# Kernel optimization log

Hardware: AMD Instinct MI355X
Metric: run time of the kernel (lower is better)

Reference implementation:

```python
import jax, jax.numpy as jnp
import numpy as np
from jax import lax

B, INP, OUP, H, W = 16, 128, 128, 56, 56
EXPAND = 6
HID = INP * EXPAND  # 768
EPS = 1e-5


def setup_inputs() -> dict:
    key = jax.random.key(0)
    ks = jax.random.split(key, 18)
    x = jax.random.normal(ks[0], (B, INP, H, W), dtype=jnp.float32)
    mask = jax.random.randint(ks[1], (B, 1, H, W), 0, 2, dtype=jnp.int32)
    w1 = jax.random.normal(ks[2], (HID, INP), dtype=jnp.float32) * 0.05
    g1 = 1.0 + 0.1 * jax.random.normal(ks[3], (HID,), dtype=jnp.float32)
    b1 = 0.1 * jax.random.normal(ks[4], (HID,), dtype=jnp.float32)
    m1 = 0.1 * jax.random.normal(ks[5], (HID,), dtype=jnp.float32)
    v1 = jax.random.uniform(ks[6], (HID,), dtype=jnp.float32) + 0.5
    wdw = jax.random.normal(ks[7], (HID, 1, 3, 3), dtype=jnp.float32) * 0.05
    g2 = 1.0 + 0.1 * jax.random.normal(ks[8], (HID,), dtype=jnp.float32)
    b2 = 0.1 * jax.random.normal(ks[9], (HID,), dtype=jnp.float32)
    m2 = 0.1 * jax.random.normal(ks[10], (HID,), dtype=jnp.float32)
    v2 = jax.random.uniform(ks[11], (HID,), dtype=jnp.float32) + 0.5
    w2 = jax.random.normal(ks[12], (OUP, HID), dtype=jnp.float32) * 0.05
    g3 = 1.0 + 0.1 * jax.random.normal(ks[13], (OUP,), dtype=jnp.float32)
    b3 = 0.1 * jax.random.normal(ks[14], (OUP,), dtype=jnp.float32)
    m3 = 0.1 * jax.random.normal(ks[15], (OUP,), dtype=jnp.float32)
    v3 = jax.random.uniform(ks[16], (OUP,), dtype=jnp.float32) + 0.5
    return dict(x=x, w1=w1, g1=g1, b1=b1, m1=m1, v1=v1, wdw=wdw,
                g2=g2, b2=b2, m2=m2, v2=v2, w2=w2,
                g3=g3, b3=b3, m3=m3, v3=v3, mask=mask)


def _bn(h, g, b, m, v):
    # inference-mode BatchNorm2d: (h - mean) * gamma/sqrt(var+eps) + beta
    scale = g / jnp.sqrt(v + EPS)
    return (h - m[None, :, None, None]) * scale[None, :, None, None] + b[None, :, None, None]


def reference(x, w1, g1, b1, m1, v1, wdw, g2, b2, m2, v2, w2, g3, b3, m3, v3, mask):
    mf = mask.astype(x.dtype)  # [B,1,H,W] binary mask ('std')
    # mask_dilate: 3x3 binary dilation (dilate_stride=1) so the depthwise conv
    # has valid neighbors for every active output pixel
    md = lax.reduce_window(mf, 0.0, lax.max, (1, 1, 3, 3), (1, 1, 1, 1), 'SAME')
    # expand 1x1 conv + BN + ReLU6, restricted to dilated mask
    h = jnp.einsum('bchw,kc->bkhw', x, w1)            # [B,HID,H,W]
    h = jnp.clip(_bn(h, g1, b1, m1, v1), 0.0, 6.0) * md
    # depthwise 3x3 conv + BN + ReLU6, restricted to std mask
    h = lax.conv_general_dilated(h, wdw, (1, 1), 'SAME',
                                 feature_group_count=HID,
                                 dimension_numbers=('NCHW', 'OIHW', 'NCHW'))
    h = jnp.clip(_bn(h, g2, b2, m2, v2), 0.0, 6.0) * mf
    # project 1x1 conv + BN (no relu), restricted to std mask
    h = jnp.einsum('bkhw,ok->bohw', h, w2)            # [B,OUP,H,W]
    h = _bn(h, g3, b3, m3, v3) * mf
    # scatter-add into identity path
    return x + h
```

## Files before the change

### kernel.cpp

```cpp
#include <hip/hip_runtime.h>
#include <hip/hip_bf16.h>

#define BATCH 16
#define INP   128
#define OUP   128
#define HH    56
#define WW    56
#define HWSZ  3136
#define HID   768
#define EPSV  1e-5f

#define SCPD  63
#define RWST  (32 * SCPD)
#define H2STR 72

typedef __attribute__((ext_vector_type(8))) short bf16x8;
typedef __attribute__((ext_vector_type(4))) float f32x4;
typedef __attribute__((ext_vector_type(2))) float f32x2;

__device__ __forceinline__ unsigned short f2b(float f) {
    unsigned u = __float_as_uint(f);
    return (unsigned short)((u + 0x7FFFu + ((u >> 16) & 1u)) >> 16);
}
__device__ __forceinline__ float blo(unsigned u){ return __uint_as_float(u << 16); }
__device__ __forceinline__ float bhi(unsigned u){ return __uint_as_float(u & 0xFFFF0000u); }
__device__ __forceinline__ unsigned pkbf(float lo, float hi) {
    unsigned r;
    asm("v_cvt_pk_bf16_f32 %0, %1, %2" : "=v"(r) : "v"(lo), "v"(hi));
    return r;
}
__device__ __forceinline__ void pkfma(f32x2& a, f32x2 b, f32x2 c) {
    asm("v_pk_fma_f32 %0, %1, %2, %0" : "+v"(a) : "v"(b), "v"(c));
}

__global__ void prep(const float* __restrict__ w1, const float* __restrict__ g1,
                     const float* __restrict__ b1, const float* __restrict__ m1, const float* __restrict__ v1,
                     const float* __restrict__ wdw, const float* __restrict__ g2,
                     const float* __restrict__ b2, const float* __restrict__ m2, const float* __restrict__ v2,
                     const float* __restrict__ w2, const float* __restrict__ g3,
                     const float* __restrict__ b3, const float* __restrict__ m3, const float* __restrict__ v3,
                     const int* __restrict__ mask,
                     unsigned short* __restrict__ w1f, unsigned short* __restrict__ w2f,
                     float* __restrict__ be1o, float* __restrict__ wdsf,
                     float* __restrict__ be2o, float* __restrict__ be3o,
                     float* __restrict__ mdf, float* __restrict__ mff)
{
    int gid = blockIdx.x * blockDim.x + threadIdx.x;
    int stp = gridDim.x * blockDim.x;
    for (int i = gid; i < HID * INP; i += stp) {
        int r = i >> 7, k = i & 127;
        float s = g1[r] * rsqrtf(v1[r] + EPSV);
        int ht = r >> 4, r16 = r & 15, ks = k >> 5, g = (k >> 3) & 3, e = k & 7;
        w1f[((((ht * 4 + ks) * 4 + g) * 16 + r16) << 3) + e] = f2b(w1[i] * s);
    }
    for (int i = gid; i < OUP * HID; i += stp) {
        int r = i / HID, k = i - r * HID;
        float s = g3[r] * rsqrtf(v3[r] + EPSV);
        int ot = r >> 4, r16 = r & 15, ch = k >> 6, ks = (k >> 5) & 1, g = (k >> 3) & 3, e = k & 7;
        int lane = g * 16 + r16;
        w2f[((((ot * 12 + ch) * 2 + ks) * 64 + lane) << 3) + e] = f2b(w2[i] * s);
    }
    for (int i = gid; i < HID; i += stp) {
        float s1 = g1[i] * rsqrtf(v1[i] + EPSV);
        be1o[i] = b1[i] - m1[i] * s1;
        float s2 = g2[i] * rsqrtf(v2[i] + EPSV);
        be2o[i] = b2[i] - m2[i] * s2;
    }
    for (int i = gid; i < HID * 9; i += stp) {
        int q = i / HID, c = i - q * HID;
        float s2 = g2[c] * rsqrtf(v2[c] + EPSV);
        wdsf[i] = wdw[c * 9 + q] * s2;
    }
    for (int i = gid; i < OUP; i += stp) {
        float s3 = g3[i] * rsqrtf(v3[i] + EPSV);
        be3o[i] = b3[i] - m3[i] * s3;
    }
    for (int i = gid; i < BATCH * HWSZ; i += stp) {
        int b = i / HWSZ, p = i - b * HWSZ;
        int y = p / WW, xx = p - y * WW;
        float mf = (float)mask[i];
        float md = 0.f;
        for (int dy = -1; dy <= 1; ++dy)
            for (int dx = -1; dx <= 1; ++dx) {
                int yy = y + dy, xc = xx + dx;
                if (yy >= 0 && yy < HH && xc >= 0 && xc < WW)
                    md = fmaxf(md, (float)mask[b * HWSZ + yy * WW + xc]);
            }
        mff[i] = mf;
        mdf[i] = md;
    }
}

__launch_bounds__(512, 4)
__global__ void k1_expand(const float* __restrict__ x,
                          const unsigned short* __restrict__ w1f,
                          const float* __restrict__ be1g,
                          const float* __restrict__ mdf,
                          unsigned* __restrict__ h1p)
{
    __shared__ unsigned short xs[128 * 128];
    const int t = threadIdx.x, lane = t & 63, wv = t >> 6;
    const int g = lane >> 4, r16 = lane & 15;
    const int pid = blockIdx.x;
    const int l = (pid & 7) * 150 + (pid >> 3);
    const int hb = l % 3;
    const int pb = (l / 3) % 25;
    const int b  = l / 75;
    const int p0 = pb * 128;
    const int whid = wv & 3;
    const int wpx  = wv >> 2;

    for (int rep = 0; rep < 8; ++rep) {
        int id = t + rep * 512;
        int px = id & 127, c4 = id >> 7;
        int p = p0 + px;
        ushort4 u; u.x = 0; u.y = 0; u.z = 0; u.w = 0;
        if (p < HWSZ) {
            const float* xp = x + ((size_t)(b * INP + c4 * 4)) * HWSZ + p;
            unsigned lo = pkbf(xp[0], xp[HWSZ]);
            unsigned hi = pkbf(xp[2 * HWSZ], xp[3 * HWSZ]);
            u.x = (unsigned short)lo; u.y = (unsigned short)(lo >> 16);
            u.z = (unsigned short)hi; u.w = (unsigned short)(hi >> 16);
        }
        *(ushort4*)&xs[px * 128 + (((c4 >> 1) ^ (px & 15)) << 3) + ((c4 & 1) << 2)] = u;
    }
    __syncthreads();

    f32x4 acc[4][4];
    #pragma unroll
    for (int mt = 0; mt < 4; ++mt)
        #pragma unroll
        for (int nt = 0; nt < 4; ++nt) {
            acc[mt][nt][0] = 0.f; acc[mt][nt][1] = 0.f;
            acc[mt][nt][2] = 0.f; acc[mt][nt][3] = 0.f;
        }
    const int hbase = hb * 256 + whid * 64;
    const int htb = hbase >> 4;

    #pragma unroll
    for (int ks = 0; ks < 4; ++ks) {
        bf16x8 af[4];
        #pragma unroll
        for (int mt = 0; mt < 4; ++mt)
            af[mt] = *(const bf16x8*)&w1f[((((htb + mt) * 4 + ks) * 64) + lane) << 3];
        #pragma unroll
        for (int nt = 0; nt < 4; ++nt) {
            int px = wpx * 64 + nt * 16 + r16;
            bf16x8 bf = *(const bf16x8*)&xs[px * 128 + (((ks * 4 + g) ^ r16) << 3)];
            #pragma unroll
            for (int mt = 0; mt < 4; ++mt)
                acc[mt][nt] = __builtin_amdgcn_mfma_f32_16x16x32_bf16(af[mt], bf, acc[mt][nt], 0, 0, 0);
        }
    }

    #pragma unroll
    for (int nt = 0; nt < 4; ++nt) {
        const int pg = p0 + wpx * 64 + nt * 16;
        if (pg >= HWSZ) continue;
        const int p = pg + r16;
        const float md = mdf[b * HWSZ + p];
        #pragma unroll
        for (int mt = 0; mt < 4; ++mt) {
            const float4 be4 = *(const float4*)&be1g[hbase + mt * 16 + g * 4];
            f32x4 a = acc[mt][nt];
            float v0 = fminf(fmaxf(a[0] + be4.x, 0.f), 6.f) * md;
            float v1 = fminf(fmaxf(a[1] + be4.y, 0.f), 6.f) * md;
            float v2 = fminf(fmaxf(a[2] + be4.z, 0.f), 6.f) * md;
            float v3 = fminf(fmaxf(a[3] + be4.w, 0.f), 6.f) * md;
            const int c2 = (hbase >> 1) + mt * 8 + g * 2;
            const size_t ad = (size_t)(b * 384 + c2) * HWSZ + p;
            h1p[ad] = pkbf(v0, v1);
            h1p[ad + HWSZ] = pkbf(v2, v3);
        }
    }
}

__launch_bounds__(512, 4)
__global__ void k23(const unsigned* __restrict__ h1p,
                    const unsigned short* __restrict__ w2f,
                    const float* __restrict__ wdsf,
                    const float* __restrict__ be2g,
                    const float* __restrict__ be3g,
                    const float* __restrict__ mff,
                    const float* __restrict__ x,
                    float* __restrict__ out)
{
    __shared__ unsigned stg[4 * RWST];
    __shared__ unsigned short h2s[112 * H2STR];
    __shared__ float mfv_[112];

    const int t = threadIdx.x, lane = t & 63, wv = t >> 6;
    const int g = lane >> 4, r16 = lane & 15;
    const int pid = blockIdx.x;
    const int l = (pid & 7) * 56 + (pid >> 3);
    const int strip = l % 28, b = l / 28;
    const int y0 = strip * 2, p0 = strip * 112;

    if (t < 112) mfv_[t] = mff[b * HWSZ + p0 + t];
    if (t >= 128 && t < 384) {
        int i = t - 128;
        int cp = i & 31, rs = (i >> 5) & 3, side = (i >> 7) & 1;
        stg[rs * RWST + cp * SCPD + (side ? 58 : 1)] = 0;
    }

    int gaddr[4], laddr[4]; bool gval[4], wval[4];
    #pragma unroll
    for (int rep = 0; rep < 4; ++rep) {
        const int id = t + rep * 512;
        const int rr  = (id * 4682) >> 16;
        const int px4 = id - rr * 14;
        const int row = rr & 3, cp = rr >> 2;
        const int gy = y0 - 1 + row;
        wval[rep] = id < 1792;
        gval[rep] = wval[rep] && gy >= 0 && gy < HH;
        gaddr[rep] = (b * 384 + cp) * HWSZ + gy * WW + px4 * 4;
        laddr[rep] = row * RWST + cp * SCPD + 2 + px4 * 4;
    }
    uint4 sreg[4];

    auto issueLoads = [&]() {
        #pragma unroll
        for (int rep = 0; rep < 4; ++rep) {
            uint4 u; u.x = 0; u.y = 0; u.z = 0; u.w = 0;
            if (gval[rep]) u = *(const uint4*)&h1p[gaddr[rep]];
            sreg[rep] = u;
            gaddr[rep] += 32 * HWSZ;
        }
    };
    auto stageWrite = [&]() {
        #pragma unroll
        for (int rep = 0; rep < 4; ++rep) {
            if (wval[rep]) {
                unsigned* s = &stg[laddr[rep]];
                s[0] = sreg[rep].x; s[1] = sreg[rep].y;
                s[2] = sreg[rep].z; s[3] = sreg[rep].w;
            }
        }
    };

    const int cp_c = t & 31, row2 = (t >> 5) & 1, q = t >> 6;
    unsigned* const h2d = (unsigned*)h2s;

    auto phaseDW = [&](int ch) {
        f32x2 acc2[7];
        {
            const float2 be2 = *(const float2*)&be2g[ch * 64 + 2 * cp_c];
            #pragma unroll
            for (int j = 0; j < 7; ++j) { acc2[j][0] = be2.x; acc2[j][1] = be2.y; }
        }
        #pragma unroll
        for (int dy = 0; dy < 3; ++dy) {
            f32x2 wt0 = *(const f32x2*)&wdsf[(dy * 3 + 0) * HID + ch * 64 + 2 * cp_c];
            f32x2 wt1 = *(const f32x2*)&wdsf[(dy * 3 + 1) * HID + ch * 64 + 2 * cp_c];
            f32x2 wt2 = *(const f32x2*)&wdsf[(dy * 3 + 2) * HID + ch * 64 + 2 * cp_c];
            const unsigned* rp = &stg[(row2 + dy) * RWST + cp_c * SCPD + 1 + q * 7];
            f32x2 p[9];
            #pragma unroll
            for (int k = 0; k < 9; ++k) {
                unsigned u = rp[k];
                p[k][0] = blo(u); p[k][1] = bhi(u);
            }
            #pragma unroll
            for (int j = 0; j < 7; ++j) {
                pkfma(acc2[j], p[j], wt0);
                pkfma(acc2[j], p[j + 1], wt1);
                pkfma(acc2[j], p[j + 2], wt2);
            }
        }
        #pragma unroll
        for (int j = 0; j < 7; ++j) {
            const int px = row2 * 56 + q * 7 + j;
            const float mv = mfv_[px];
            float vL = __builtin_amdgcn_fmed3f(acc2[j][0], 0.f, 6.f) * mv;
            float vH = __builtin_amdgcn_fmed3f(acc2[j][1], 0.f, 6.f) * mv;
            h2d[px * 36 + (((cp_c >> 2) ^ (px & 7)) << 2) + (cp_c & 3)] = pkbf(vL, vH);
        }
    };

    f32x4 pacc[7];
    #pragma unroll
    for (int nt = 0; nt < 7; ++nt) {
        pacc[nt][0] = 0.f; pacc[nt][1] = 0.f; pacc[nt][2] = 0.f; pacc[nt][3] = 0.f;
    }

    auto phaseP = [&](int ch) {
        #pragma unroll
        for (int ks = 0; ks < 2; ++ks) {
            const bf16x8 pw = *(const bf16x8*)&w2f[((((wv * 12 + ch) * 2 + ks) * 64) + lane) << 3];
            #pragma unroll
            for (int nt = 0; nt < 7; ++nt) {
                const int px = nt * 16 + r16;
                const bf16x8 hb = *(const bf16x8*)&h2s[px * H2STR + (((ks * 4 + g) ^ (px & 7)) << 3)];
                pacc[nt] = __builtin_amdgcn_mfma_f32_16x16x32_bf16(pw, hb, pacc[nt], 0, 0, 0);
            }
        }
    };

    issueLoads();
    stageWrite();
    __syncthreads();
    for (int ch = 0; ch < 12; ++ch) {
        if (ch + 1 < 12) issueLoads();
        phaseDW(ch);
        __syncthreads();
        if (ch + 1 < 12) stageWrite();
        phaseP(ch);
        __syncthreads();
    }

    {
        const int ob = wv * 16 + g * 4;
        const float4 be4 = *(const float4*)&be3g[ob];
        #pragma unroll
        for (int nt = 0; nt < 7; ++nt) {
            const int px = nt * 16 + r16;
            const float mv = mfv_[px];
            const size_t base = (size_t)(b * OUP + ob) * HWSZ + p0 + px;
            out[base]            = x[base]            + (pacc[nt][0] + be4.x) * mv;
            out[base + HWSZ]     = x[base + HWSZ]     + (pacc[nt][1] + be4.y) * mv;
            out[base + 2 * HWSZ] = x[base + 2 * HWSZ] + (pacc[nt][2] + be4.z) * mv;
            out[base + 3 * HWSZ] = x[base + 3 * HWSZ] + (pacc[nt][3] + be4.w) * mv;
        }
    }
}

extern "C" void kernel_launch(void* const* d_in, const int* in_sizes, int n_in,
                              void* d_out, int out_size, void* d_ws, size_t ws_size,
                              hipStream_t stream) {
    (void)in_sizes; (void)n_in; (void)out_size; (void)ws_size;
    const float* x   = (const float*)d_in[0];
    const float* w1  = (const float*)d_in[1];
    const float* g1  = (const float*)d_in[2];
    const float* b1  = (const float*)d_in[3];
    const float* m1  = (const float*)d_in[4];
    const float* v1  = (const float*)d_in[5];
    const float* wdw = (const float*)d_in[6];
    const float* g2  = (const float*)d_in[7];
    const float* b2  = (const float*)d_in[8];
    const float* m2  = (const float*)d_in[9];
    const float* v2  = (const float*)d_in[10];
    const float* w2  = (const float*)d_in[11];
    const float* g3  = (const float*)d_in[12];
    const float* b3  = (const float*)d_in[13];
    const float* m3  = (const float*)d_in[14];
    const float* v3  = (const float*)d_in[15];
    const int*  mask = (const int*)d_in[16];
    float* out = (float*)d_out;

    char* ws = (char*)d_ws;
    unsigned short* w1f = (unsigned short*)ws;
    unsigned short* w2f = (unsigned short*)(ws + 196608);
    float* be1o = (float*)(ws + 393216);
    float* wdsf = (float*)(ws + 396288);
    float* be2o = (float*)(ws + 423936);
    float* be3o = (float*)(ws + 427008);
    float* mdf  = (float*)(ws + 427520);
    float* mff  = (float*)(ws + 628224);
    unsigned* h1p = (unsigned*)(ws + 828928);

    prep<<<256, 256, 0, stream>>>(w1, g1, b1, m1, v1, wdw, g2, b2, m2, v2,
                                  w2, g3, b3, m3, v3, mask,
                                  w1f, w2f, be1o, wdsf, be2o, be3o, mdf, mff);
    k1_expand<<<dim3(1200), 512, 0, stream>>>(x, w1f, be1o, mdf, h1p);
    k23<<<dim3(448), 512, 0, stream>>>(h1p, w2f, wdsf, be2o, be3o, mff, x, out);
}
```

Baseline: 89.94 us.

## Transpose depthwise staging to pixel-major and pad LDS strides against bank conflicts

The depthwise staging buffer in k23 changes from channel-major rows to pixel-major rows with a padded stride of 33 words. Each thread now issues seven 8-byte global loads instead of four 16-byte ones. The XOR swizzles on the h2s tile and on the expand kernel's x tile are replaced or supplemented by odd row padding (strides of 66 and 130 halfwords), aiming to cut LDS bank conflicts. The trade-off is that 128-bit LDS reads now start at addresses that are not 16-byte aligned, which can split accesses or hurt correctness, and the narrower global loads may lower memory efficiency.

```diff
diff --git a/kernel.cpp b/kernel.cpp
--- a/kernel.cpp
+++ b/kernel.cpp
@@ -10,9 +10,10 @@
 #define HID   768
 #define EPSV  1e-5f
 
-#define SCPD  63
-#define RWST  (32 * SCPD)
-#define H2STR 72
+#define PXST  33
+#define RWST2 1920
+#define H2STR 66
+#define XSTR  130
 
 typedef __attribute__((ext_vector_type(8))) short bf16x8;
 typedef __attribute__((ext_vector_type(4))) float f32x4;
@@ -98,7 +99,7 @@
                           const float* __restrict__ mdf,
                           unsigned* __restrict__ h1p)
 {
-    __shared__ unsigned short xs[128 * 128];
+    __shared__ unsigned short xs[128 * XSTR];
     const int t = threadIdx.x, lane = t & 63, wv = t >> 6;
     const int g = lane >> 4, r16 = lane & 15;
     const int pid = blockIdx.x;
@@ -122,7 +123,7 @@
             u.x = (unsigned short)lo; u.y = (unsigned short)(lo >> 16);
             u.z = (unsigned short)hi; u.w = (unsigned short)(hi >> 16);
         }
-        *(ushort4*)&xs[px * 128 + (((c4 >> 1) ^ (px & 15)) << 3) + ((c4 & 1) << 2)] = u;
+        *(ushort4*)&xs[px * XSTR + (((c4 >> 1) ^ (px & 15)) << 3) + ((c4 & 1) << 2)] = u;
     }
     __syncthreads();
 
@@ -146,7 +147,7 @@
         #pragma unroll
         for (int nt = 0; nt < 4; ++nt) {
             int px = wpx * 64 + nt * 16 + r16;
-            bf16x8 bf = *(const bf16x8*)&xs[px * 128 + (((ks * 4 + g) ^ r16) << 3)];
+            bf16x8 bf = *(const bf16x8*)&xs[px * XSTR + (((ks * 4 + g) ^ r16) << 3)];
             #pragma unroll
             for (int mt = 0; mt < 4; ++mt)
                 acc[mt][nt] = __builtin_amdgcn_mfma_f32_16x16x32_bf16(af[mt], bf, acc[mt][nt], 0, 0, 0);
@@ -185,7 +186,7 @@
                     const float* __restrict__ x,
                     float* __restrict__ out)
 {
-    __shared__ unsigned stg[4 * RWST];
+    __shared__ unsigned stg[4 * RWST2];
     __shared__ unsigned short h2s[112 * H2STR];
     __shared__ float mfv_[112];
 
@@ -199,42 +200,38 @@
     if (t < 112) mfv_[t] = mff[b * HWSZ + p0 + t];
     if (t >= 128 && t < 384) {
         int i = t - 128;
-        int cp = i & 31, rs = (i >> 5) & 3, side = (i >> 7) & 1;
-        stg[rs * RWST + cp * SCPD + (side ? 58 : 1)] = 0;
-    }
-
-    int gaddr[4], laddr[4]; bool gval[4], wval[4];
-    #pragma unroll
-    for (int rep = 0; rep < 4; ++rep) {
+        int cp = i & 31, row = (i >> 5) & 3, side = (i >> 7) & 1;
+        stg[row * RWST2 + (side ? 57 * PXST : 0) + cp] = 0;
+    }
+
+    int gaddr[7], laddr[7]; bool gval[7];
+    #pragma unroll
+    for (int rep = 0; rep < 7; ++rep) {
         const int id = t + rep * 512;
-        const int rr  = (id * 4682) >> 16;
-        const int px4 = id - rr * 14;
-        const int row = rr & 3, cp = rr >> 2;
+        const int rr = (id * 2341) >> 16;
+        const int p2 = id - rr * 28;
+        const int cp = rr >> 2, row = rr & 3;
         const int gy = y0 - 1 + row;
-        wval[rep] = id < 1792;
-        gval[rep] = wval[rep] && gy >= 0 && gy < HH;
-        gaddr[rep] = (b * 384 + cp) * HWSZ + gy * WW + px4 * 4;
-        laddr[rep] = row * RWST + cp * SCPD + 2 + px4 * 4;
-    }
-    uint4 sreg[4];
+        gval[rep] = gy >= 0 && gy < HH;
+        gaddr[rep] = (b * 384 + cp) * HWSZ + gy * WW + 2 * p2;
+        laddr[rep] = row * RWST2 + (2 * p2 + 1) * PXST + cp;
+    }
+    uint2 sreg[7];
 
     auto issueLoads = [&]() {
         #pragma unroll
-        for (int rep = 0; rep < 4; ++rep) {
-            uint4 u; u.x = 0; u.y = 0; u.z = 0; u.w = 0;
-            if (gval[rep]) u = *(const uint4*)&h1p[gaddr[rep]];
+        for (int rep = 0; rep < 7; ++rep) {
+            uint2 u; u.x = 0; u.y = 0;
+            if (gval[rep]) u = *(const uint2*)&h1p[gaddr[rep]];
             sreg[rep] = u;
             gaddr[rep] += 32 * HWSZ;
         }
     };
     auto stageWrite = [&]() {
         #pragma unroll
-        for (int rep = 0; rep < 4; ++rep) {
-            if (wval[rep]) {
-                unsigned* s = &stg[laddr[rep]];
-                s[0] = sreg[rep].x; s[1] = sreg[rep].y;
-                s[2] = sreg[rep].z; s[3] = sreg[rep].w;
-            }
+        for (int rep = 0; rep < 7; ++rep) {
+            stg[laddr[rep]] = sreg[rep].x;
+            stg[laddr[rep] + PXST] = sreg[rep].y;
         }
     };
 
@@ -253,11 +250,11 @@
             f32x2 wt0 = *(const f32x2*)&wdsf[(dy * 3 + 0) * HID + ch * 64 + 2 * cp_c];
             f32x2 wt1 = *(const f32x2*)&wdsf[(dy * 3 + 1) * HID + ch * 64 + 2 * cp_c];
             f32x2 wt2 = *(const f32x2*)&wdsf[(dy * 3 + 2) * HID + ch * 64 + 2 * cp_c];
-            const unsigned* rp = &stg[(row2 + dy) * RWST + cp_c * SCPD + 1 + q * 7];
+            const unsigned* rp = &stg[(row2 + dy) * RWST2 + (q * 7) * PXST + cp_c];
             f32x2 p[9];
             #pragma unroll
             for (int k = 0; k < 9; ++k) {
-                unsigned u = rp[k];
+                unsigned u = rp[k * PXST];
                 p[k][0] = blo(u); p[k][1] = bhi(u);
             }
             #pragma unroll
@@ -273,7 +270,7 @@
             const float mv = mfv_[px];
             float vL = __builtin_amdgcn_fmed3f(acc2[j][0], 0.f, 6.f) * mv;
             float vH = __builtin_amdgcn_fmed3f(acc2[j][1], 0.f, 6.f) * mv;
-            h2d[px * 36 + (((cp_c >> 2) ^ (px & 7)) << 2) + (cp_c & 3)] = pkbf(vL, vH);
+            h2d[px * 33 + cp_c] = pkbf(vL, vH);
         }
     };
 
@@ -290,7 +287,7 @@
             #pragma unroll
             for (int nt = 0; nt < 7; ++nt) {
                 const int px = nt * 16 + r16;
-                const bf16x8 hb = *(const bf16x8*)&h2s[px * H2STR + (((ks * 4 + g) ^ (px & 7)) << 3)];
+                const bf16x8 hb = *(const bf16x8*)&h2s[px * H2STR + (ks * 4 + g) * 8];
                 pacc[nt] = __builtin_amdgcn_mfma_f32_16x16x32_bf16(pw, hb, pacc[nt], 0, 0, 0);
             }
         }
```

New measurement: 101.7 us. +13.1%, slower.
